# Kernel optimization log

Measured on AMD Instinct MI355X. Metric: run time of the kernel, lower is better.

## Reference

```python
import jax, jax.numpy as jnp
import numpy as np

B, T, H = 16, 512, 768
S = 32            # gold spans per example
L = 50            # max_span_len -> candidate ends per span
NT = 3            # num_types
HS = 4 * H        # span repr size


def setup_inputs() -> dict:
    key = jax.random.key(0)
    ks = jax.random.split(key, 8)
    h = jax.random.normal(ks[0], (B, T, H), dtype=jnp.float32)
    attention_mask = jnp.ones((B, T), dtype=jnp.int32)
    starts = jax.random.randint(ks[1], (B, S), 1, 400).astype(jnp.int32)
    lens = jax.random.randint(ks[2], (B, S), 0, L).astype(jnp.int32)
    ends = starts + lens                      # <= 448 < last_tok=510
    types = jax.random.randint(ks[3], (B, S), 0, NT).astype(jnp.int32)
    W1 = jax.random.normal(ks[4], (HS, HS), dtype=jnp.float32) * (1.0 / np.sqrt(HS))
    b1 = jnp.zeros((HS,), dtype=jnp.float32)
    w_score = jax.random.normal(ks[5], (HS,), dtype=jnp.float32) * (1.0 / np.sqrt(HS))
    b_score = jnp.zeros((1,), dtype=jnp.float32)
    W_type = jax.random.normal(ks[6], (HS, NT), dtype=jnp.float32) * (1.0 / np.sqrt(HS))
    b_type = jnp.zeros((NT,), dtype=jnp.float32)
    return {"h": h, "attention_mask": attention_mask, "span_starts": starts,
            "span_ends": ends, "span_types": types, "W1": W1, "b1": b1,
            "w_score": w_score, "b_score": b_score, "W_type": W_type, "b_type": b_type}


def _span_loss(h, attention_mask, span_starts, span_ends, span_types,
               W1, b1, w_score, b_score, W_type, b_type, type_loss_weight=1.0):
    cls = h[:, 0]                                              # [B,H]
    # prefix sums for O(1) segment means: pre[b,t] = sum h[b,0:t]
    pre = jnp.concatenate([jnp.zeros((B, 1, H), h.dtype), jnp.cumsum(h, axis=1)], axis=1)

    valid_len = attention_mask.sum(axis=1)                     # [B]
    last_tok = jnp.maximum(1, valid_len - 2)                   # [B]

    s = span_starts                                            # [B,S]
    e_gold = span_ends
    gold_idx = e_gold - s                                      # [B,S]
    lt = last_tok[:, None]
    span_valid = (s >= 1) & (s <= lt) & (e_gold >= s) & (e_gold <= lt) & (gold_idx < L)

    e_max = jnp.minimum(s + L - 1, lt)                         # [B,S]
    p = s[..., None] + jnp.arange(L, dtype=s.dtype)            # [B,S,L] candidate ends
    cand_valid = p <= e_max[..., None]

    sc = jnp.clip(s, 0, T - 1)
    pc = jnp.clip(p, 0, T - 1)
    bi2 = jnp.arange(B)[:, None]
    bi3 = jnp.arange(B)[:, None, None]

    h_start = h[bi2, sc]                                       # [B,S,H]
    h_end = h[bi3, pc]                                         # [B,S,L,H]
    seg_len = jnp.maximum(p - s[..., None] + 1, 1).astype(h.dtype)
    h_mean = (pre[bi3, pc + 1] - pre[bi2, sc][:, :, None]) / seg_len[..., None]

    repr_ = jnp.concatenate([
        jnp.broadcast_to(h_start[:, :, None], (B, S, L, H)),
        h_end,
        h_mean,
        jnp.broadcast_to(cls[:, None, None], (B, S, L, H)),
    ], axis=-1)                                                # [B,S,L,4H]

    h1 = jax.nn.gelu(jnp.einsum('bslh,hd->bsld', repr_, W1) + b1, approximate=False)
    scores = jnp.einsum('bsld,d->bsl', h1, w_score) + b_score[0]      # [B,S,L]
    type_logits = jnp.einsum('bsld,dk->bslk', h1, W_type) + b_type    # [B,S,L,NT]

    # end-index CE over valid candidate ends
    masked = jnp.where(cand_valid, scores, jnp.float32(-1e9))
    logp_end = jax.nn.log_softmax(masked, axis=-1)             # [B,S,L]
    gi = jnp.clip(gold_idx, 0, L - 1)
    end_loss = -jnp.take_along_axis(logp_end, gi[..., None], axis=-1)[..., 0]  # [B,S]

    # type CE at the gold end index
    tl_gold = jnp.take_along_axis(type_logits, gi[..., None, None], axis=2)[:, :, 0]  # [B,S,NT]
    logp_t = jax.nn.log_softmax(tl_gold, axis=-1)
    tg = jnp.clip(span_types, 0, NT - 1)
    type_loss = -jnp.take_along_axis(logp_t, tg[..., None], axis=-1)[..., 0]  # [B,S]

    vmask = span_valid.astype(h.dtype)
    n_seg = vmask.sum()
    denom = jnp.maximum(n_seg, 1.0)
    loss_end = jnp.where(n_seg > 0, (end_loss * vmask).sum() / denom, 0.0)
    loss_type = jnp.where(n_seg > 0, (type_loss * vmask).sum() / denom, 0.0)
    return loss_end + type_loss_weight * loss_type


def reference(h, attention_mask, span_starts, span_ends, span_types,
              W1, b1, w_score, b_score, W_type, b_type):
    return _span_loss(h, attention_mask, span_starts, span_ends, span_types,
                      W1, b1, w_score, b_score, W_type, b_type)
```

## Files before the change

kernel.cpp:

```cpp
#include <hip/hip_runtime.h>
#include <hip/hip_bf16.h>
#include <math.h>

#define B_ 16
#define T_ 512
#define H_ 768
#define S_ 32
#define L_ 50
#define NT_ 3
#define HS_ 3072
#define CH_ 8
#define CT_ 64

#define XROWS 8192
#define YBASE 8192
#define GBASE 16512
#define XYROWS 16400
#define AROWS 17152

typedef __attribute__((ext_vector_type(8))) short short8;
typedef __attribute__((ext_vector_type(16))) float float16v;

__device__ __forceinline__ unsigned short f2bf(float f) {
    __hip_bfloat16 b = __float2bfloat16(f);
    return *(unsigned short*)&b;
}
__device__ __forceinline__ float bf2f(unsigned short u) {
    union { unsigned int i; float f; } v; v.i = ((unsigned int)u) << 16; return v.f;
}
__device__ __forceinline__ void load_lds16(const void* g, void* l) {
    __builtin_amdgcn_global_load_lds((__attribute__((address_space(1))) void*)g,
                                     (__attribute__((address_space(3))) void*)l, 16, 0, 0);
}

__device__ __forceinline__ float gelu_exact(float v) {
    float a = fabsf(v) * 0.70710678118654752f;
    float t = __builtin_amdgcn_rcpf(fmaf(a, 0.47047f, 1.0f));
    float poly = t * fmaf(t, fmaf(t, 0.7478556f, -0.0958798f), 0.3480242f);
    float e = __builtin_amdgcn_exp2f(a * a * -1.4426950408889634f);
    float erfa = fmaf(-poly, e, 1.0f);
    float erfv = copysignf(erfa, v);
    return 0.5f * v * (1.0f + erfv);
}

__global__ __launch_bounds__(256) void cumsum_pass1(const float* __restrict__ h,
                                                    float* __restrict__ partial) {
    int idx = blockIdx.x * 256 + threadIdx.x;
    int hd = idx % H_; int t = idx / H_; int ch = t % CH_; int b = t / CH_;
    const float* hp = h + ((size_t)b * T_ + ch * CT_) * H_ + hd;
    float acc = 0.f;
#pragma unroll 8
    for (int tt = 0; tt < CT_; tt++) acc += hp[(size_t)tt * H_];
    partial[idx] = acc;
}

__global__ __launch_bounds__(256) void cumsum_pass3(const float* __restrict__ h,
                                                    const float* __restrict__ partial,
                                                    __hip_bfloat16* __restrict__ Ab) {
    int idx = blockIdx.x * 256 + threadIdx.x;
    int hd = idx % H_; int t = idx / H_; int ch = t % CH_; int b = t / CH_;
    float acc = 0.f;
#pragma unroll
    for (int c = 0; c < CH_; c++)
        if (c < ch) acc += partial[((size_t)b * CH_ + c) * H_ + hd];
    int row0 = b * T_ + ch * CT_;
    const float* hp = h + (size_t)row0 * H_ + hd;
    __hip_bfloat16* hb = Ab + (size_t)row0 * H_ + hd;
    __hip_bfloat16* pp = Ab + ((size_t)(YBASE + b * (T_ + 1) + ch * CT_ + 1)) * H_ + hd;
    if (ch == 0) Ab[((size_t)(YBASE + b * (T_ + 1))) * H_ + hd] = __float2bfloat16(0.f);
#pragma unroll 8
    for (int tt = 0; tt < CT_; tt++) {
        float hv = hp[(size_t)tt * H_];
        hb[(size_t)tt * H_] = __float2bfloat16(hv);
        acc += hv;
        pp[(size_t)tt * H_] = __float2bfloat16(acc);
    }
}

__global__ void gather_kernel(const float* __restrict__ h,
                              const int* __restrict__ starts,
                              __hip_bfloat16* __restrict__ Ab) {
    int r = blockIdx.x;
    int src_row;
    if (r < B_ * S_) {
        int b = r / S_;
        int sv = starts[r];
        int sc = min(max(sv, 0), T_ - 1);
        src_row = b * T_ + sc;
    } else {
        int b = r - B_ * S_;
        src_row = b * T_;
    }
    __hip_bfloat16* dst = Ab + (size_t)(GBASE + r) * H_;
    for (int j = threadIdx.x; j < H_; j += 256)
        dst[j] = __float2bfloat16(h[(size_t)src_row * H_ + j]);
}

__global__ __launch_bounds__(256) void transpose_w(const float* __restrict__ W1,
                                                   __hip_bfloat16* __restrict__ Wt) {
    __shared__ float tile[64][65];
    int n0 = blockIdx.x * 64, k0 = blockIdx.y * 64;
    int c = threadIdx.x & 63, r0 = threadIdx.x >> 6;
#pragma unroll
    for (int i = 0; i < 16; i++) {
        int r = r0 + i * 4;
        tile[r][c] = W1[(size_t)(k0 + r) * HS_ + n0 + c];
    }
    __syncthreads();
    int p = k0 / H_, kl = k0 % H_;
    __hip_bfloat16* out = Wt + (size_t)p * HS_ * H_;
#pragma unroll
    for (int i = 0; i < 16; i++) {
        int r = r0 + i * 4;
        out[(size_t)(n0 + r) * H_ + kl + c] = __float2bfloat16(tile[c][r]);
    }
}

__global__ __launch_bounds__(256) void mfma_gemm(const __hip_bfloat16* __restrict__ Ab,
                                                 const __hip_bfloat16* __restrict__ Wt,
                                                 __hip_bfloat16* __restrict__ XY,
                                                 float* __restrict__ ST,
                                                 float* __restrict__ CC) {
    constexpr int K = H_;
    __shared__ __hip_bfloat16 As[2][128][32];
    __shared__ __hip_bfloat16 Bs[2][128][32];
    int tid = threadIdx.x;
    int wave = tid >> 6, lane = tid & 63;
    int m0 = blockIdx.x * 128, n0 = blockIdx.y * 128;
    int wm = (wave & 1) * 64, wn = (wave >> 1) * 64;

    const __hip_bfloat16* Bt;
    if (m0 < XROWS)            Bt = Wt + (size_t)1 * HS_ * H_;
    else if (m0 < GBASE)       Bt = Wt + (size_t)2 * HS_ * H_;
    else if (m0 < GBASE + 512) Bt = Wt;
    else                       Bt = Wt + (size_t)3 * HS_ * H_;

    float16v acc[2][2] = {};

    int l31 = lane & 31, lh = lane >> 5;

    for (int k0 = 0; k0 < K; k0 += 64) {
        __syncthreads();
#pragma unroll
        for (int i = 0; i < 4; i++) {
            int c = i * 256 + wave * 64 + lane;
            int hh = c >> 9, row = (c >> 2) & 127, kc = c & 3;
            size_t go = (size_t)row * K + k0 + hh * 32 + kc * 8;
            char* ldsbase = (char*)As + (size_t)(i * 256 + wave * 64) * 16;
            load_lds16(Ab + (size_t)m0 * K + go, ldsbase);
            char* ldsbaseB = (char*)Bs + (size_t)(i * 256 + wave * 64) * 16;
            load_lds16(Bt + (size_t)n0 * K + go, ldsbaseB);
        }
        __syncthreads();

        const short* Asp = (const short*)As;
        const short* Bsp = (const short*)Bs;
#pragma unroll
        for (int kk = 0; kk < 4; kk++) {
            int hh = kk >> 1;
            int ko = (kk & 1) * 16 + lh * 8;
            short8 af[2], bf[2];
#pragma unroll
            for (int mi = 0; mi < 2; mi++)
                af[mi] = *(const short8*)&Asp[hh * 4096 + (wm + mi * 32 + l31) * 32 + ko];
#pragma unroll
            for (int ni = 0; ni < 2; ni++)
                bf[ni] = *(const short8*)&Bsp[hh * 4096 + (wn + ni * 32 + l31) * 32 + ko];
#pragma unroll
            for (int mi = 0; mi < 2; mi++)
#pragma unroll
                for (int ni = 0; ni < 2; ni++)
                    acc[mi][ni] = __builtin_amdgcn_mfma_f32_32x32x16_bf16(
                        af[mi], bf[ni], acc[mi][ni], 0, 0, 0);
        }
    }

#pragma unroll
    for (int mi = 0; mi < 2; mi++) {
#pragma unroll
        for (int ni = 0; ni < 2; ni++) {
            int n = n0 + wn + ni * 32 + l31;
#pragma unroll
            for (int r = 0; r < 16; r++) {
                int m = m0 + wm + mi * 32 + (r & 3) + 8 * (r >> 2) + 4 * lh;
                float v = acc[mi][ni][r];
                if (m < XYROWS) {
                    XY[(size_t)m * HS_ + n] = __float2bfloat16(v);
                } else if (m >= GBASE && m < GBASE + 512) {
                    ST[(size_t)(m - GBASE) * HS_ + n] = v;
                } else if (m >= GBASE + 512 && m < GBASE + 528) {
                    CC[(size_t)(m - GBASE - 512) * HS_ + n] = v;
                }
            }
        }
    }
}

__global__ __launch_bounds__(256) void c0_kernel(const float4* __restrict__ ST,
                                                 const float4* __restrict__ CC,
                                                 const float4* __restrict__ b1,
                                                 ushort4* __restrict__ c0b) {
    int i = blockIdx.x * 256 + threadIdx.x;
    int row = i / (HS_ / 4);
    int b = row >> 5;
    int c4 = i % (HS_ / 4);
    float4 s = ST[i], c = CC[b * (HS_ / 4) + c4], bb = b1[c4];
    ushort4 o;
    o.x = f2bf(s.x + c.x + bb.x);
    o.y = f2bf(s.y + c.y + bb.y);
    o.z = f2bf(s.z + c.z + bb.z);
    o.w = f2bf(s.w + c.w + bb.w);
    c0b[i] = o;
}

__global__ __launch_bounds__(256) void combine_kernel(
    const unsigned short* __restrict__ c0, const __hip_bfloat16* __restrict__ XY,
    const float* __restrict__ w_score, const float* __restrict__ b_score,
    const float* __restrict__ W_type,
    const int* __restrict__ starts, const int* __restrict__ ends,
    float* __restrict__ scores, float* __restrict__ tgold) {
    int bs = blockIdx.x;
    int b = bs >> 5;
    int wave = threadIdx.x >> 6, lane = threadIdx.x & 63;
    int l = blockIdx.y * 4 + wave;
    if (l >= L_) return;
    int sv = starts[bs], ev = ends[bs];
    int gi = min(max(ev - sv, 0), L_ - 1);
    int sc = min(max(sv, 0), T_ - 1);
    int p = sv + l;
    int pc = min(max(p, 0), T_ - 1);
    float invlen = 1.0f / (float)(l + 1);
    bool isg = (l == gi);

    const unsigned short* Xr = (const unsigned short*)(XY + (size_t)(b * T_ + pc) * HS_);
    const unsigned short* Yp = (const unsigned short*)(XY + (size_t)(YBASE + b * (T_ + 1) + pc + 1) * HS_);
    const unsigned short* Ys = (const unsigned short*)(XY + (size_t)(YBASE + b * (T_ + 1) + sc) * HS_);
    const unsigned short* c0r = c0 + (size_t)bs * HS_;

    float local = 0.f, t0 = 0.f, t1 = 0.f, t2 = 0.f;
#pragma unroll
    for (int j = 0; j < 6; j++) {
        int d = j * 512 + lane * 8;
        short8 xv = *(const short8*)(Xr + d);
        short8 yv = *(const short8*)(Yp + d);
        short8 sv8 = *(const short8*)(Ys + d);
        short8 cv8 = *(const short8*)(c0r + d);
        float4 wa = *(const float4*)(w_score + d);
        float4 wb = *(const float4*)(w_score + d + 4);
        float wv[8] = {wa.x, wa.y, wa.z, wa.w, wb.x, wb.y, wb.z, wb.w};
#pragma unroll
        for (int q = 0; q < 8; q++) {
            float x = bf2f(((const unsigned short*)&xv)[q]);
            float y = bf2f(((const unsigned short*)&yv)[q]);
            float ys = bf2f(((const unsigned short*)&sv8)[q]);
            float cv = bf2f(((const unsigned short*)&cv8)[q]);
            float v = fmaf(y - ys, invlen, cv) + x;
            float g = gelu_exact(v);
            local = fmaf(g, wv[q], local);
            if (isg) {
                t0 = fmaf(g, W_type[(d + q) * NT_ + 0], t0);
                t1 = fmaf(g, W_type[(d + q) * NT_ + 1], t1);
                t2 = fmaf(g, W_type[(d + q) * NT_ + 2], t2);
            }
        }
    }
#pragma unroll
    for (int off = 32; off >= 1; off >>= 1) local += __shfl_down(local, off);
    if (lane == 0) scores[(size_t)bs * L_ + l] = local + b_score[0];
    if (isg) {
#pragma unroll
        for (int off = 32; off >= 1; off >>= 1) {
            t0 += __shfl_down(t0, off);
            t1 += __shfl_down(t1, off);
            t2 += __shfl_down(t2, off);
        }
        if (lane == 0) {
            tgold[bs * NT_ + 0] = t0;
            tgold[bs * NT_ + 1] = t1;
            tgold[bs * NT_ + 2] = t2;
        }
    }
}

__global__ __launch_bounds__(512) void loss_kernel(
    const float* __restrict__ scores, const float* __restrict__ tgold,
    const int* __restrict__ mask, const int* __restrict__ starts,
    const int* __restrict__ ends, const int* __restrict__ types,
    const float* __restrict__ b_type, float* __restrict__ out) {
    __shared__ int svl[B_];
    __shared__ float r[3][8];
    int tid = threadIdx.x;
    int b = tid / S_;
    if (tid < B_) svl[tid] = 0;
    __syncthreads();
    {
        int part = 0;
        const int* mp = mask + tid * 16;
#pragma unroll
        for (int i = 0; i < 16; i++) part += mp[i];
        atomicAdd(&svl[tid / (T_ / 16)], part);
    }
    __syncthreads();
    int vl = svl[b];
    int lt = max(1, vl - 2);
    int sv = starts[tid], ev = ends[tid];
    int gold = ev - sv;
    bool valid = (sv >= 1) && (sv <= lt) && (ev >= sv) && (ev <= lt) && (gold < L_);
    int emax = min(sv + L_ - 1, lt);
    const float* sp = scores + (size_t)tid * L_;
    float m = -1e30f;
    for (int l = 0; l < L_; l++) {
        float v = (sv + l <= emax) ? sp[l] : -1e9f;
        m = fmaxf(m, v);
    }
    float sum = 0.f;
    for (int l = 0; l < L_; l++) {
        float v = (sv + l <= emax) ? sp[l] : -1e9f;
        sum += expf(v - m);
    }
    int gi = min(max(gold, 0), L_ - 1);
    float vg = (sv + gi <= emax) ? sp[gi] : -1e9f;
    float end_loss = (m + logf(sum)) - vg;

    float t0 = tgold[tid * 3 + 0] + b_type[0];
    float t1 = tgold[tid * 3 + 1] + b_type[1];
    float t2 = tgold[tid * 3 + 2] + b_type[2];
    float tm = fmaxf(t0, fmaxf(t1, t2));
    float tsum = expf(t0 - tm) + expf(t1 - tm) + expf(t2 - tm);
    int tg = min(max(types[tid], 0), NT_ - 1);
    float tv = (tg == 0) ? t0 : ((tg == 1) ? t1 : t2);
    float type_loss = (tm + logf(tsum)) - tv;

    float ve = valid ? end_loss : 0.f;
    float vt = valid ? type_loss : 0.f;
    float vc = valid ? 1.f : 0.f;
    for (int off = 32; off >= 1; off >>= 1) {
        ve += __shfl_down(ve, off);
        vt += __shfl_down(vt, off);
        vc += __shfl_down(vc, off);
    }
    if ((tid & 63) == 0) {
        int w = tid >> 6;
        r[0][w] = ve; r[1][w] = vt; r[2][w] = vc;
    }
    __syncthreads();
    if (tid == 0) {
        float se = 0, st = 0, n = 0;
        for (int w = 0; w < 8; w++) { se += r[0][w]; st += r[1][w]; n += r[2][w]; }
        float denom = fmaxf(n, 1.f);
        out[0] = (n > 0.f) ? (se / denom + st / denom) : 0.f;
    }
}

extern "C" void kernel_launch(void* const* d_in, const int* in_sizes, int n_in,
                              void* d_out, int out_size, void* d_ws, size_t ws_size,
                              hipStream_t stream) {
    const float* h       = (const float*)d_in[0];
    const int*   mask    = (const int*)d_in[1];
    const int*   starts  = (const int*)d_in[2];
    const int*   ends    = (const int*)d_in[3];
    const int*   types   = (const int*)d_in[4];
    const float* W1      = (const float*)d_in[5];
    const float* b1      = (const float*)d_in[6];
    const float* w_score = (const float*)d_in[7];
    const float* b_score = (const float*)d_in[8];
    const float* W_type  = (const float*)d_in[9];
    const float* b_type  = (const float*)d_in[10];
    float* out = (float*)d_out;

    char* ws = (char*)d_ws;
    size_t off = 0;
    __hip_bfloat16* Ab = (__hip_bfloat16*)(ws + off); off += (size_t)AROWS * H_ * 2;
    __hip_bfloat16* XY = (__hip_bfloat16*)(ws + off); off += (size_t)XYROWS * HS_ * 2;
    __hip_bfloat16* Wt = (__hip_bfloat16*)(ws + off); off += (size_t)4 * HS_ * H_ * 2;
    float* ST     = (float*)(ws + off);               off += (size_t)512 * HS_ * 4;
    float* CC     = (float*)(ws + off);               off += (size_t)16 * HS_ * 4;
    unsigned short* c0b = (unsigned short*)(ws + off); off += (size_t)512 * HS_ * 2;
    float* scores = (float*)(ws + off);               off += (size_t)B_ * S_ * L_ * 4;
    float* tgold  = (float*)(ws + off);               off += (size_t)B_ * S_ * NT_ * 4;
    float* partial = (float*)XY;

    hipLaunchKernelGGL(cumsum_pass1, dim3(B_ * CH_ * H_ / 256), dim3(256), 0, stream, h, partial);
    hipLaunchKernelGGL(cumsum_pass3, dim3(B_ * CH_ * H_ / 256), dim3(256), 0, stream, h, partial, Ab);
    hipLaunchKernelGGL(gather_kernel, dim3(B_ * S_ + B_), dim3(256), 0, stream, h, starts, Ab);
    hipLaunchKernelGGL(transpose_w, dim3(48, 48), dim3(256), 0, stream, W1, Wt);

    hipLaunchKernelGGL(mfma_gemm, dim3(AROWS / 128, 24), dim3(256), 0, stream,
                       Ab, Wt, XY, ST, CC);
    hipLaunchKernelGGL(c0_kernel, dim3(512 * HS_ / 4 / 256), dim3(256), 0, stream,
                       (const float4*)ST, (const float4*)CC, (const float4*)b1,
                       (ushort4*)c0b);
    hipLaunchKernelGGL(combine_kernel, dim3(B_ * S_, 13), dim3(256), 0, stream,
                       c0b, XY, w_score, b_score, W_type, starts, ends, scores, tgold);
    hipLaunchKernelGGL(loss_kernel, dim3(1), dim3(512), 0, stream,
                       scores, tgold, mask, starts, ends, types, b_type, out);
}
```

Baseline: 364.5 us.

## Vectorize cumsum passes, swizzle GEMM LDS layout, and swap GEMM grid order

The cumsum kernels now use float4 loads and packed bf16x4 stores, with more chunks (32×16 instead of 8×64) so more threads run and each does less serial work. The GEMM applies an XOR swizzle to the LDS chunk index to reduce bank conflicts on fragment reads. It also swaps the grid axes so consecutive blocks share an A tile across N, which should improve L2 reuse. The extra cumsum chunks make pass3 read more partials per thread.

New measurement: 343.0 us. 1.06x faster.

```diff
diff --git a/kernel.cpp b/kernel.cpp
--- a/kernel.cpp
+++ b/kernel.cpp
@@ -9,8 +9,8 @@
 #define L_ 50
 #define NT_ 3
 #define HS_ 3072
-#define CH_ 8
-#define CT_ 64
+#define CH_ 32
+#define CT_ 16
 
 #define XROWS 8192
 #define YBASE 8192
@@ -31,6 +31,10 @@
 __device__ __forceinline__ void load_lds16(const void* g, void* l) {
     __builtin_amdgcn_global_load_lds((__attribute__((address_space(1))) void*)g,
                                      (__attribute__((address_space(3))) void*)l, 16, 0, 0);
+}
+__device__ __forceinline__ ushort4 pack4(float4 v) {
+    ushort4 o; o.x = f2bf(v.x); o.y = f2bf(v.y); o.z = f2bf(v.z); o.w = f2bf(v.w);
+    return o;
 }
 
 __device__ __forceinline__ float gelu_exact(float v) {
@@ -43,37 +47,47 @@
     return 0.5f * v * (1.0f + erfv);
 }
 
-__global__ __launch_bounds__(256) void cumsum_pass1(const float* __restrict__ h,
-                                                    float* __restrict__ partial) {
+__global__ __launch_bounds__(256) void cumsum_pass1(const float4* __restrict__ h4,
+                                                    float4* __restrict__ partial) {
     int idx = blockIdx.x * 256 + threadIdx.x;
-    int hd = idx % H_; int t = idx / H_; int ch = t % CH_; int b = t / CH_;
-    const float* hp = h + ((size_t)b * T_ + ch * CT_) * H_ + hd;
-    float acc = 0.f;
-#pragma unroll 8
-    for (int tt = 0; tt < CT_; tt++) acc += hp[(size_t)tt * H_];
+    int hd4 = idx % 192; int t = idx / 192; int ch = t % CH_; int b = t / CH_;
+    const float4* hp = h4 + ((size_t)b * T_ + ch * CT_) * 192 + hd4;
+    float4 acc = {0.f, 0.f, 0.f, 0.f};
+#pragma unroll
+    for (int tt = 0; tt < CT_; tt++) {
+        float4 v = hp[(size_t)tt * 192];
+        acc.x += v.x; acc.y += v.y; acc.z += v.z; acc.w += v.w;
+    }
     partial[idx] = acc;
 }
 
-__global__ __launch_bounds__(256) void cumsum_pass3(const float* __restrict__ h,
-                                                    const float* __restrict__ partial,
-                                                    __hip_bfloat16* __restrict__ Ab) {
+__global__ __launch_bounds__(256) void cumsum_pass3(const float4* __restrict__ h4,
+                                                    const float4* __restrict__ partial,
+                                                    ushort4* __restrict__ Ab4) {
     int idx = blockIdx.x * 256 + threadIdx.x;
-    int hd = idx % H_; int t = idx / H_; int ch = t % CH_; int b = t / CH_;
-    float acc = 0.f;
-#pragma unroll
-    for (int c = 0; c < CH_; c++)
-        if (c < ch) acc += partial[((size_t)b * CH_ + c) * H_ + hd];
+    int hd4 = idx % 192; int t = idx / 192; int ch = t % CH_; int b = t / CH_;
+    float4 acc = {0.f, 0.f, 0.f, 0.f};
+#pragma unroll
+    for (int c = 0; c < CH_; c++) {
+        if (c < ch) {
+            float4 v = partial[((size_t)b * CH_ + c) * 192 + hd4];
+            acc.x += v.x; acc.y += v.y; acc.z += v.z; acc.w += v.w;
+        }
+    }
     int row0 = b * T_ + ch * CT_;
-    const float* hp = h + (size_t)row0 * H_ + hd;
-    __hip_bfloat16* hb = Ab + (size_t)row0 * H_ + hd;
-    __hip_bfloat16* pp = Ab + ((size_t)(YBASE + b * (T_ + 1) + ch * CT_ + 1)) * H_ + hd;
-    if (ch == 0) Ab[((size_t)(YBASE + b * (T_ + 1))) * H_ + hd] = __float2bfloat16(0.f);
-#pragma unroll 8
+    const float4* hp = h4 + (size_t)row0 * 192 + hd4;
+    ushort4* hb = Ab4 + (size_t)row0 * 192 + hd4;
+    ushort4* pp = Ab4 + ((size_t)(YBASE + b * (T_ + 1) + ch * CT_ + 1)) * 192 + hd4;
+    if (ch == 0) {
+        ushort4 z = {0, 0, 0, 0};
+        Ab4[((size_t)(YBASE + b * (T_ + 1))) * 192 + hd4] = z;
+    }
+#pragma unroll
     for (int tt = 0; tt < CT_; tt++) {
-        float hv = hp[(size_t)tt * H_];
-        hb[(size_t)tt * H_] = __float2bfloat16(hv);
-        acc += hv;
-        pp[(size_t)tt * H_] = __float2bfloat16(acc);
+        float4 hv = hp[(size_t)tt * 192];
+        hb[(size_t)tt * 192] = pack4(hv);
+        acc.x += hv.x; acc.y += hv.y; acc.z += hv.z; acc.w += hv.w;
+        pp[(size_t)tt * 192] = pack4(acc);
     }
 }
 
@@ -122,11 +136,11 @@
                                                  float* __restrict__ ST,
                                                  float* __restrict__ CC) {
     constexpr int K = H_;
-    __shared__ __hip_bfloat16 As[2][128][32];
-    __shared__ __hip_bfloat16 Bs[2][128][32];
+    __shared__ __hip_bfloat16 As[2 * 128 * 32];
+    __shared__ __hip_bfloat16 Bs[2 * 128 * 32];
     int tid = threadIdx.x;
     int wave = tid >> 6, lane = tid & 63;
-    int m0 = blockIdx.x * 128, n0 = blockIdx.y * 128;
+    int n0 = blockIdx.x * 128, m0 = blockIdx.y * 128;
     int wm = (wave & 1) * 64, wn = (wave >> 1) * 64;
 
     const __hip_bfloat16* Bt;
@@ -143,13 +157,14 @@
         __syncthreads();
 #pragma unroll
         for (int i = 0; i < 4; i++) {
-            int c = i * 256 + wave * 64 + lane;
-            int hh = c >> 9, row = (c >> 2) & 127, kc = c & 3;
-            size_t go = (size_t)row * K + k0 + hh * 32 + kc * 8;
-            char* ldsbase = (char*)As + (size_t)(i * 256 + wave * 64) * 16;
-            load_lds16(Ab + (size_t)m0 * K + go, ldsbase);
-            char* ldsbaseB = (char*)Bs + (size_t)(i * 256 + wave * 64) * 16;
-            load_lds16(Bt + (size_t)n0 * K + go, ldsbaseB);
+            int cid = i * 256 + wave * 64 + lane;
+            int hh = cid >> 9, row = (cid >> 2) & 127, pc = cid & 3;
+            int lc = pc ^ ((row >> 1) & 3);
+            size_t go = (size_t)row * K + k0 + hh * 32 + lc * 8;
+            load_lds16(Ab + (size_t)m0 * K + go,
+                       (char*)As + (size_t)(i * 256 + wave * 64) * 16);
+            load_lds16(Bt + (size_t)n0 * K + go,
+                       (char*)Bs + (size_t)(i * 256 + wave * 64) * 16);
         }
         __syncthreads();
 
@@ -158,14 +173,20 @@
 #pragma unroll
         for (int kk = 0; kk < 4; kk++) {
             int hh = kk >> 1;
-            int ko = (kk & 1) * 16 + lh * 8;
+            int lc = 2 * (kk & 1) + lh;
             short8 af[2], bf[2];
 #pragma unroll
-            for (int mi = 0; mi < 2; mi++)
-                af[mi] = *(const short8*)&Asp[hh * 4096 + (wm + mi * 32 + l31) * 32 + ko];
-#pragma unroll
-            for (int ni = 0; ni < 2; ni++)
-                bf[ni] = *(const short8*)&Bsp[hh * 4096 + (wn + ni * 32 + l31) * 32 + ko];
+            for (int mi = 0; mi < 2; mi++) {
+                int row = wm + mi * 32 + l31;
+                int pc = lc ^ ((row >> 1) & 3);
+                af[mi] = *(const short8*)&Asp[(hh * 512 + row * 4 + pc) * 8];
+            }
+#pragma unroll
+            for (int ni = 0; ni < 2; ni++) {
+                int row = wn + ni * 32 + l31;
+                int pc = lc ^ ((row >> 1) & 3);
+                bf[ni] = *(const short8*)&Bsp[(hh * 512 + row * 4 + pc) * 8];
+            }
 #pragma unroll
             for (int mi = 0; mi < 2; mi++)
 #pragma unroll
@@ -205,12 +226,8 @@
     int b = row >> 5;
     int c4 = i % (HS_ / 4);
     float4 s = ST[i], c = CC[b * (HS_ / 4) + c4], bb = b1[c4];
-    ushort4 o;
-    o.x = f2bf(s.x + c.x + bb.x);
-    o.y = f2bf(s.y + c.y + bb.y);
-    o.z = f2bf(s.z + c.z + bb.z);
-    o.w = f2bf(s.w + c.w + bb.w);
-    c0b[i] = o;
+    float4 v = {s.x + c.x + bb.x, s.y + c.y + bb.y, s.z + c.z + bb.z, s.w + c.w + bb.w};
+    c0b[i] = pack4(v);
 }
 
 __global__ __launch_bounds__(256) void combine_kernel(
@@ -378,14 +395,16 @@
     unsigned short* c0b = (unsigned short*)(ws + off); off += (size_t)512 * HS_ * 2;
     float* scores = (float*)(ws + off);               off += (size_t)B_ * S_ * L_ * 4;
     float* tgold  = (float*)(ws + off);               off += (size_t)B_ * S_ * NT_ * 4;
-    float* partial = (float*)XY;
-
-    hipLaunchKernelGGL(cumsum_pass1, dim3(B_ * CH_ * H_ / 256), dim3(256), 0, stream, h, partial);
-    hipLaunchKernelGGL(cumsum_pass3, dim3(B_ * CH_ * H_ / 256), dim3(256), 0, stream, h, partial, Ab);
+    float4* partial = (float4*)XY;
+
+    hipLaunchKernelGGL(cumsum_pass1, dim3(B_ * CH_ * 192 / 256), dim3(256), 0, stream,
+                       (const float4*)h, partial);
+    hipLaunchKernelGGL(cumsum_pass3, dim3(B_ * CH_ * 192 / 256), dim3(256), 0, stream,
+                       (const float4*)h, partial, (ushort4*)Ab);
     hipLaunchKernelGGL(gather_kernel, dim3(B_ * S_ + B_), dim3(256), 0, stream, h, starts, Ab);
     hipLaunchKernelGGL(transpose_w, dim3(48, 48), dim3(256), 0, stream, W1, Wt);
 
-    hipLaunchKernelGGL(mfma_gemm, dim3(AROWS / 128, 24), dim3(256), 0, stream,
+    hipLaunchKernelGGL(mfma_gemm, dim3(24, AROWS / 128), dim3(256), 0, stream,
                        Ab, Wt, XY, ST, CC);
     hipLaunchKernelGGL(c0_kernel, dim3(512 * HS_ / 4 / 256), dim3(256), 0, stream,
                        (const float4*)ST, (const float4*)CC, (const float4*)b1,
```
